# Kernel tuning notes

Measured on AMD Instinct MI355X. Metric: run time of the kernel, lower is better.

## Reference

```python
import jax, jax.numpy as jnp
import numpy as np

B, S, D, H = 4, 2048, 1024, 16
DH = D // H  # 64
EPS = 1e-5


def setup_inputs() -> dict:
    key = jax.random.key(0)
    ks = jax.random.split(key, 6)
    scale = 0.02
    return {
        "x": jax.random.normal(ks[0], (B, S, D), dtype=jnp.float32),
        "Wq": jax.random.normal(ks[1], (H, D, DH), dtype=jnp.float32) * scale,
        "Wk": jax.random.normal(ks[2], (H, D, DH), dtype=jnp.float32) * scale,
        "Wv": jax.random.normal(ks[3], (H, D, DH), dtype=jnp.float32) * scale,
        "Wo": jax.random.normal(ks[4], (D, D), dtype=jnp.float32) * scale,
        "bo": jnp.zeros((D,), dtype=jnp.float32),
        "gamma": jnp.ones((D,), dtype=jnp.float32),
        "beta": jnp.zeros((D,), dtype=jnp.float32),
    }


def reference(x, Wq, Wk, Wv, Wo, bo, gamma, beta):
    # Per-head projections, stacked across heads: [B,H,S,DH]
    q = jnp.einsum("bsd,hdk->bhsk", x, Wq)
    k = jnp.einsum("bsd,hdk->bhsk", x, Wk)
    v = jnp.einsum("bsd,hdk->bhsk", x, Wv)
    inv_scale = 1.0 / jnp.sqrt(jnp.float32(DH))  # key.size(-1) == head_dim
    scores = jnp.einsum("bhqk,bhsk->bhqs", q, k) * inv_scale  # [B,H,S,S]
    attn = jax.nn.softmax(scores, axis=-1)
    ctx = jnp.einsum("bhqs,bhsk->bhqk", attn, v)  # [B,H,S,DH]
    # concat heads -> [B,S,D]
    concat = jnp.transpose(ctx, (0, 2, 1, 3)).reshape(B, S, D)
    proj = concat @ Wo + bo  # fc_out (Wo stored as [in,out])
    added = proj + x  # residual add
    mu = jnp.mean(added, axis=-1, keepdims=True)
    var = jnp.mean(jnp.square(added - mu), axis=-1, keepdims=True)
    normed = (added - mu) * jax.lax.rsqrt(var + EPS)
    return normed * gamma + beta
```

## Files before the change

### kernel.cpp

```cpp
#include <hip/hip_runtime.h>
#include <hip/hip_bf16.h>
#include <stdint.h>

#define DEV __device__ __forceinline__

typedef short s16x8 __attribute__((ext_vector_type(8)));
typedef float f32x4 __attribute__((ext_vector_type(4)));
typedef int i32x4 __attribute__((ext_vector_type(4)));

DEV void async_load16(const void* g, void* l) {
  __builtin_amdgcn_global_load_lds((void __attribute__((address_space(1)))*)(g),
                                   (void __attribute__((address_space(3)))*)(l),
                                   16, 0, 0);
}

DEV unsigned pack_bf16x2(float a, float b) {
  __hip_bfloat162 h = __float22bfloat162_rn(make_float2(a, b));
  union { __hip_bfloat162 h2; unsigned u; } cv;
  cv.h2 = h;
  return cv.u;
}

__global__ __launch_bounds__(256) void cast_x_kernel(const float* __restrict__ in,
                                                     __hip_bfloat16* __restrict__ out, int n4) {
  int i = blockIdx.x * 256 + threadIdx.x;
  if (i >= n4) return;
  float4 v = ((const float4*)in)[i];
  alignas(8) __hip_bfloat16 t[4] = {__float2bfloat16(v.x), __float2bfloat16(v.y),
                                    __float2bfloat16(v.z), __float2bfloat16(v.w)};
  *(uint2*)(out + (size_t)i * 4) = *(const uint2*)t;
}

__global__ __launch_bounds__(256) void transpose_cast_kernel(const float* __restrict__ src,
                                                             __hip_bfloat16* __restrict__ dst,
                                                             int R, int C, float scale) {
  __shared__ float tile[64][65];
  const int r0 = blockIdx.x * 64, c0 = blockIdx.y * 64, bt = blockIdx.z;
  const int tc = threadIdx.x & 63, tr = threadIdx.x >> 6;
  const float* sp = src + (size_t)bt * R * C;
#pragma unroll
  for (int rr = 0; rr < 64; rr += 4)
    tile[tr + rr][tc] = sp[(size_t)(r0 + tr + rr) * C + c0 + tc];
  __syncthreads();
  __hip_bfloat16* dp = dst + (size_t)bt * R * C;
#pragma unroll
  for (int rr = 0; rr < 64; rr += 4) {
    int cc = tr + rr;
    dp[(size_t)(c0 + cc) * R + r0 + tc] = __float2bfloat16(tile[tc][cc] * scale);
  }
}

__global__ __launch_bounds__(256) void qkv_transpose_kernel(const float* __restrict__ Wq,
                                                            const float* __restrict__ Wk,
                                                            const float* __restrict__ Wv,
                                                            __hip_bfloat16* __restrict__ dst,
                                                            float qscale) {
  __shared__ float tile[64][65];
  const int z = blockIdx.z, which = z >> 4, bt = z & 15;
  const int r0 = blockIdx.x * 64;
  const int tc = threadIdx.x & 63, tr = threadIdx.x >> 6;
  const float* src = (which == 0) ? Wq : (which == 1) ? Wk : Wv;
  const float scale = (which == 0) ? qscale : 1.0f;
  const float* sp = src + (size_t)bt * 1024 * 64;
#pragma unroll
  for (int rr = 0; rr < 64; rr += 4)
    tile[tr + rr][tc] = sp[(size_t)(r0 + tr + rr) * 64 + tc];
  __syncthreads();
  __hip_bfloat16* dp = dst + (size_t)z * 1024 * 64;
#pragma unroll
  for (int rr = 0; rr < 64; rr += 4) {
    int cc = tr + rr;
    dp[(size_t)(cc)*1024 + r0 + tc] = __float2bfloat16(tile[tc][cc] * scale);
  }
}

template <int MODE>
__global__ __launch_bounds__(256) void gemm128(const __hip_bfloat16* __restrict__ A,
                                               const __hip_bfloat16* __restrict__ Bt,
                                               void* __restrict__ out0,
                                               void* __restrict__ out1,
                                               void* __restrict__ out2,
                                               const float* __restrict__ bias,
                                               const float* __restrict__ resid,
                                               int M, int N, int K) {
  __shared__ __hip_bfloat16 As[128 * 32];
  __shared__ __hip_bfloat16 Bs[128 * 32];
  const int tid = threadIdx.x;
  const int lane = tid & 63, w = tid >> 6;
  const int lr = lane & 15, lq = lane >> 4;
  const int wm = w >> 1, wn = w & 1;
  const int m0 = blockIdx.y * 128, n0 = blockIdx.x * 128;

  const f32x4 fz = {0.f, 0.f, 0.f, 0.f};
  f32x4 acc[4][4];
#pragma unroll
  for (int i = 0; i < 4; i++)
#pragma unroll
    for (int j = 0; j < 4; j++) acc[i][j] = fz;

  const int kiters = K >> 5;
  for (int kt = 0; kt < kiters; kt++) {
    __syncthreads();
#pragma unroll
    for (int r = 0; r < 2; r++) {
      const int c = r * 256 + tid;
      const int row = c >> 2, kc = c & 3;
      async_load16((const short*)A + (size_t)(m0 + row) * K + kt * 32 + kc * 8,
                   (char*)As + (r * 256 + (tid & 0xC0)) * 16);
      async_load16((const short*)Bt + (size_t)(n0 + row) * K + kt * 32 + kc * 8,
                   (char*)Bs + (r * 256 + (tid & 0xC0)) * 16);
    }
    __syncthreads();
    const short* Ap = (const short*)As;
    const short* Bp = (const short*)Bs;
    s16x8 av[4], bv[4];
#pragma unroll
    for (int i = 0; i < 4; i++)
      av[i] = *(const s16x8*)(Ap + (wm * 64 + i * 16 + lr) * 32 + lq * 8);
#pragma unroll
    for (int j = 0; j < 4; j++)
      bv[j] = *(const s16x8*)(Bp + (wn * 64 + j * 16 + lr) * 32 + lq * 8);
#pragma unroll
    for (int i = 0; i < 4; i++)
#pragma unroll
      for (int j = 0; j < 4; j++)
        acc[i][j] = __builtin_amdgcn_mfma_f32_16x16x32_bf16(av[i], bv[j], acc[i][j], 0, 0, 0);
  }

  if constexpr (MODE == 0) {
    if (n0 < 2048) {
      __hip_bfloat16* dst01 = (__hip_bfloat16*)((n0 < 1024) ? out0 : out1);
#pragma unroll
      for (int i = 0; i < 4; i++)
#pragma unroll
        for (int j = 0; j < 4; j++)
#pragma unroll
          for (int r = 0; r < 4; r++) {
            const int row = m0 + wm * 64 + i * 16 + lq * 4 + r;
            const int col = n0 + wn * 64 + j * 16 + lr;
            const int bb = row >> 11, s = row & 2047;
            const int colq = col & 1023;
            dst01[((((size_t)bb * 16 + (colq >> 6)) * 2048 + s) << 6) + (col & 63)] =
                __float2bfloat16(acc[i][j][r]);
          }
    } else {
#pragma unroll
      for (int i = 0; i < 4; i++)
#pragma unroll
        for (int j = 0; j < 4; j++) {
          const int row0 = m0 + wm * 64 + i * 16 + lq * 4;
          const int col = (n0 - 2048) + wn * 64 + j * 16 + lr;
          const int bb = row0 >> 11, s0 = row0 & 2047;
          alignas(8) __hip_bfloat16 t4[4] = {
              __float2bfloat16(acc[i][j][0]), __float2bfloat16(acc[i][j][1]),
              __float2bfloat16(acc[i][j][2]), __float2bfloat16(acc[i][j][3])};
          *(uint2*)((__hip_bfloat16*)out2 + (size_t)bb * 2097152 + (size_t)col * 2048 + s0) =
              *(const uint2*)t4;
        }
    }
  } else {
#pragma unroll
    for (int i = 0; i < 4; i++)
#pragma unroll
      for (int j = 0; j < 4; j++)
#pragma unroll
        for (int r = 0; r < 4; r++) {
          const int row = m0 + wm * 64 + i * 16 + lq * 4 + r;
          const int col = n0 + wn * 64 + j * 16 + lr;
          const size_t idx = (size_t)row * 1024 + col;
          ((float*)out0)[idx] = acc[i][j][r] + bias[col] + resid[idx];
        }
  }
}

__global__ __launch_bounds__(128, 2) void flash_kernel(const __hip_bfloat16* __restrict__ Qg,
                                                       const __hip_bfloat16* __restrict__ Kg,
                                                       const __hip_bfloat16* __restrict__ Vtg,
                                                       __hip_bfloat16* __restrict__ Og) {
  __shared__ alignas(16) char smem[32768];
  float* xch = (float*)smem;
  const int tid = threadIdx.x;
  const int lane = tid & 63, w = tid >> 6;
  const int lr = lane & 15, lq = lane >> 4;
  const int hb = blockIdx.x, qt = blockIdx.y;
  const int h = hb >> 2, b = hb & 3;
  const size_t bh = (size_t)b * 16 + h;
  const short* Qbase = (const short*)Qg + (bh * 2048 + (size_t)qt * 64) * 64;
  const short* Kbh = (const short*)Kg + bh * 2048 * 64;
  const short* Vbh = (const short*)Vtg + bh * 64 * 2048;

  const int rbase = (lr >> 2) * 8 + (lr & 3);
  const int gk = lr & 7;

  s16x8 qb[4][2];
#pragma unroll
  for (int nt = 0; nt < 4; nt++)
#pragma unroll
    for (int ks = 0; ks < 2; ks++)
      qb[nt][ks] = *(const s16x8*)(Qbase + (nt * 16 + lr) * 64 + ks * 32 + lq * 8);

  s16x8 vones;
#pragma unroll
  for (int e = 0; e < 8; e++) vones[e] = (short)0x3F80;

  const f32x4 fz = {0.f, 0.f, 0.f, 0.f};
  f32x4 o[4][4];
  f32x4 ol[4];
#pragma unroll
  for (int i = 0; i < 4; i++) {
    ol[i] = fz;
#pragma unroll
    for (int j = 0; j < 4; j++) o[i][j] = fz;
  }

  auto stage = [&](int sel, int kb) {
    char* Kl = smem + sel * 16384;
    char* Vl = Kl + 8192;
    const short* Ksrc = Kbh + kb * 64 * 64;
#pragma unroll
    for (int r = 0; r < 4; r++) {
      int c = r * 128 + tid;
      int row = c >> 3, ck = c & 7;
      int g = (row & 3) | (((row >> 3) & 1) << 2);
      async_load16(Ksrc + row * 64 + (ck ^ g) * 8, Kl + (r * 128 + (tid & 64)) * 16);
    }
#pragma unroll
    for (int r = 0; r < 4; r++) {
      int c = r * 128 + tid;
      int row = c >> 3, ck = c & 7;
      async_load16(Vbh + (size_t)row * 2048 + kb * 64 + ((ck ^ (row & 7))) * 8,
                   Vl + (r * 128 + (tid & 64)) * 16);
    }
  };

  stage(0, 0);
  __syncthreads();

  for (int kb = 0; kb < 32; kb++) {
    const int cur = kb & 1;
    if (kb + 1 < 32) stage(cur ^ 1, kb + 1);

    const short* Kp = (const short*)(smem + cur * 16384);
    const short* Vp = (const short*)(smem + cur * 16384 + 8192);

    union { i32x4 i; s16x8 s; } pa[4];
#pragma unroll
    for (int mt = 0; mt < 2; mt++) {
      const int kvrow = w * 32 + mt * 4 + rbase;
      s16x8 kf0 = *(const s16x8*)(Kp + kvrow * 64 + (((0 * 4 + lq) ^ gk)) * 8);
      s16x8 kf1 = *(const s16x8*)(Kp + kvrow * 64 + (((1 * 4 + lq) ^ gk)) * 8);
#pragma unroll
      for (int nt = 0; nt < 4; nt++) {
        f32x4 st = fz;
        st = __builtin_amdgcn_mfma_f32_16x16x32_bf16(kf0, qb[nt][0], st, 0, 0, 0);
        st = __builtin_amdgcn_mfma_f32_16x16x32_bf16(kf1, qb[nt][1], st, 0, 0, 0);
        float e0 = __builtin_amdgcn_exp2f(st[0]);
        float e1 = __builtin_amdgcn_exp2f(st[1]);
        float e2 = __builtin_amdgcn_exp2f(st[2]);
        float e3 = __builtin_amdgcn_exp2f(st[3]);
        pa[nt].i[mt * 2 + 0] = (int)pack_bf16x2(e0, e1);
        pa[nt].i[mt * 2 + 1] = (int)pack_bf16x2(e2, e3);
      }
    }
    __builtin_amdgcn_s_setprio(1);
#pragma unroll
    for (int nt = 0; nt < 4; nt++)
      ol[nt] = __builtin_amdgcn_mfma_f32_16x16x32_bf16(pa[nt].s, vones, ol[nt], 0, 0, 0);
#pragma unroll
    for (int ndh = 0; ndh < 4; ndh++) {
      int vrow = ndh * 16 + lr;
      s16x8 vb = *(const s16x8*)(Vp + vrow * 64 + (((w * 4 + lq) ^ (vrow & 7))) * 8);
#pragma unroll
      for (int nt = 0; nt < 4; nt++)
        o[nt][ndh] = __builtin_amdgcn_mfma_f32_16x16x32_bf16(pa[nt].s, vb, o[nt][ndh], 0, 0, 0);
    }
    __builtin_amdgcn_s_setprio(0);

    __syncthreads();
  }

  __syncthreads();
  if (w == 0) {
#pragma unroll
    for (int j = 0; j < 2; j++) {
#pragma unroll
      for (int ndh = 0; ndh < 4; ndh++)
        *(f32x4*)(xch + 0 * 2560 + (j * 4 + ndh) * 256 + lane * 4) = o[2 + j][ndh];
      *(f32x4*)(xch + 0 * 2560 + 2048 + j * 256 + lane * 4) = ol[2 + j];
    }
  } else {
#pragma unroll
    for (int j = 0; j < 2; j++) {
#pragma unroll
      for (int ndh = 0; ndh < 4; ndh++)
        *(f32x4*)(xch + 1 * 2560 + (j * 4 + ndh) * 256 + lane * 4) = o[0 + j][ndh];
      *(f32x4*)(xch + 1 * 2560 + 2048 + j * 256 + lane * 4) = ol[0 + j];
    }
  }
  __syncthreads();
  if (w == 0) {
#pragma unroll
    for (int j = 0; j < 2; j++) {
#pragma unroll
      for (int ndh = 0; ndh < 4; ndh++)
        o[0 + j][ndh] += *(const f32x4*)(xch + 1 * 2560 + (j * 4 + ndh) * 256 + lane * 4);
      f32x4 lt = ol[0 + j] + *(const f32x4*)(xch + 1 * 2560 + 2048 + j * 256 + lane * 4);
#pragma unroll
      for (int r = 0; r < 4; r++) {
        float inv = __builtin_amdgcn_rcpf(lt[r]);
        int rowg = qt * 64 + (0 + j) * 16 + lq * 4 + r;
#pragma unroll
        for (int ndh = 0; ndh < 4; ndh++)
          Og[((size_t)b * 2048 + rowg) * 1024 + h * 64 + ndh * 16 + lr] =
              __float2bfloat16(o[0 + j][ndh][r] * inv);
      }
    }
  } else {
#pragma unroll
    for (int j = 0; j < 2; j++) {
#pragma unroll
      for (int ndh = 0; ndh < 4; ndh++)
        o[2 + j][ndh] += *(const f32x4*)(xch + 0 * 2560 + (j * 4 + ndh) * 256 + lane * 4);
      f32x4 lt = ol[2 + j] + *(const f32x4*)(xch + 0 * 2560 + 2048 + j * 256 + lane * 4);
#pragma unroll
      for (int r = 0; r < 4; r++) {
        float inv = __builtin_amdgcn_rcpf(lt[r]);
        int rowg = qt * 64 + (2 + j) * 16 + lq * 4 + r;
#pragma unroll
        for (int ndh = 0; ndh < 4; ndh++)
          Og[((size_t)b * 2048 + rowg) * 1024 + h * 64 + ndh * 16 + lr] =
              __float2bfloat16(o[2 + j][ndh][r] * inv);
      }
    }
  }
}

__global__ __launch_bounds__(256) void ln_kernel(const float* __restrict__ tmp,
                                                 const float* __restrict__ gamma,
                                                 const float* __restrict__ beta,
                                                 float* __restrict__ out) {
  const int row = blockIdx.x, tid = threadIdx.x;
  const int lane = tid & 63, w = tid >> 6;
  const float* rp = tmp + (size_t)row * 1024;
  float4 v = ((const float4*)rp)[tid];
  float s = v.x + v.y + v.z + v.w;
  float ss = v.x * v.x + v.y * v.y + v.z * v.z + v.w * v.w;
#pragma unroll
  for (int off = 32; off >= 1; off >>= 1) {
    s += __shfl_xor(s, off);
    ss += __shfl_xor(ss, off);
  }
  __shared__ float red[8];
  if (lane == 0) {
    red[w] = s;
    red[4 + w] = ss;
  }
  __syncthreads();
  s = red[0] + red[1] + red[2] + red[3];
  ss = red[4] + red[5] + red[6] + red[7];
  const float mu = s * (1.0f / 1024.0f);
  const float var = ss * (1.0f / 1024.0f) - mu * mu;
  const float rstd = rsqrtf(var + 1e-5f);
  float4 g = ((const float4*)gamma)[tid];
  float4 be = ((const float4*)beta)[tid];
  float4 ov;
  ov.x = (v.x - mu) * rstd * g.x + be.x;
  ov.y = (v.y - mu) * rstd * g.y + be.y;
  ov.z = (v.z - mu) * rstd * g.z + be.z;
  ov.w = (v.w - mu) * rstd * g.w + be.w;
  ((float4*)(out + (size_t)row * 1024))[tid] = ov;
}

extern "C" void kernel_launch(void* const* d_in, const int* in_sizes, int n_in,
                              void* d_out, int out_size, void* d_ws, size_t ws_size,
                              hipStream_t stream) {
  (void)in_sizes; (void)n_in; (void)out_size; (void)ws_size;
  const float* x = (const float*)d_in[0];
  const float* Wq = (const float*)d_in[1];
  const float* Wk = (const float*)d_in[2];
  const float* Wv = (const float*)d_in[3];
  const float* Wo = (const float*)d_in[4];
  const float* bo = (const float*)d_in[5];
  const float* gamma = (const float*)d_in[6];
  const float* beta = (const float*)d_in[7];
  float* out = (float*)d_out;
  char* ws = (char*)d_ws;

  __hip_bfloat16* xb = (__hip_bfloat16*)(ws + 0);
  __hip_bfloat16* wqkvT = (__hip_bfloat16*)(ws + 16777216);
  __hip_bfloat16* woT = (__hip_bfloat16*)(ws + 23068672);
  __hip_bfloat16* Q = (__hip_bfloat16*)(ws + 25165824);
  __hip_bfloat16* Kt = (__hip_bfloat16*)(ws + 41943040);
  __hip_bfloat16* Vt = (__hip_bfloat16*)(ws + 58720256);
  __hip_bfloat16* cc = (__hip_bfloat16*)(ws + 75497472);
  float* tmp = (float*)(ws + 25165824);

  cast_x_kernel<<<8192, 256, 0, stream>>>(x, xb, 2097152);
  qkv_transpose_kernel<<<dim3(16, 1, 48), 256, 0, stream>>>(Wq, Wk, Wv, wqkvT,
                                                            0.125f * 1.44269504088896f);
  transpose_cast_kernel<<<dim3(16, 16, 1), 256, 0, stream>>>(Wo, woT, 1024, 1024, 1.0f);

  gemm128<0><<<dim3(24, 64), 256, 0, stream>>>(xb, wqkvT, Q, Kt, Vt, nullptr, nullptr,
                                               8192, 3072, 1024);

  flash_kernel<<<dim3(64, 32), 128, 0, stream>>>(Q, Kt, Vt, cc);

  gemm128<2><<<dim3(8, 64), 256, 0, stream>>>(cc, woT, tmp, nullptr, nullptr, bo, x,
                                              8192, 1024, 1024);
  ln_kernel<<<8192, 256, 0, stream>>>(tmp, gamma, beta, out);
}
```

Baseline: 309.1 us.

## Split flash attention work across four waves per block instead of two

```diff
diff --git a/kernel.cpp b/kernel.cpp
--- a/kernel.cpp
+++ b/kernel.cpp
@@ -173,7 +173,7 @@
   }
 }
 
-__global__ __launch_bounds__(128, 2) void flash_kernel(const __hip_bfloat16* __restrict__ Qg,
+__global__ __launch_bounds__(256, 4) void flash_kernel(const __hip_bfloat16* __restrict__ Qg,
                                                        const __hip_bfloat16* __restrict__ Kg,
                                                        const __hip_bfloat16* __restrict__ Vtg,
                                                        __hip_bfloat16* __restrict__ Og) {
@@ -182,6 +182,8 @@
   const int tid = threadIdx.x;
   const int lane = tid & 63, w = tid >> 6;
   const int lr = lane & 15, lq = lane >> 4;
+  const int qp = w >> 1;
+  const int kvh = w & 1;
   const int hb = blockIdx.x, qt = blockIdx.y;
   const int h = hb >> 2, b = hb & 3;
   const size_t bh = (size_t)b * 16 + h;
@@ -192,22 +194,23 @@
   const int rbase = (lr >> 2) * 8 + (lr & 3);
   const int gk = lr & 7;
 
-  s16x8 qb[4][2];
-#pragma unroll
-  for (int nt = 0; nt < 4; nt++)
+  s16x8 qb[2][2];
+#pragma unroll
+  for (int ntl = 0; ntl < 2; ntl++)
 #pragma unroll
     for (int ks = 0; ks < 2; ks++)
-      qb[nt][ks] = *(const s16x8*)(Qbase + (nt * 16 + lr) * 64 + ks * 32 + lq * 8);
+      qb[ntl][ks] =
+          *(const s16x8*)(Qbase + ((qp * 2 + ntl) * 16 + lr) * 64 + ks * 32 + lq * 8);
 
   s16x8 vones;
 #pragma unroll
   for (int e = 0; e < 8; e++) vones[e] = (short)0x3F80;
 
   const f32x4 fz = {0.f, 0.f, 0.f, 0.f};
-  f32x4 o[4][4];
-  f32x4 ol[4];
-#pragma unroll
-  for (int i = 0; i < 4; i++) {
+  f32x4 o[2][4];
+  f32x4 ol[2];
+#pragma unroll
+  for (int i = 0; i < 2; i++) {
     ol[i] = fz;
 #pragma unroll
     for (int j = 0; j < 4; j++) o[i][j] = fz;
@@ -218,18 +221,18 @@
     char* Vl = Kl + 8192;
     const short* Ksrc = Kbh + kb * 64 * 64;
 #pragma unroll
-    for (int r = 0; r < 4; r++) {
-      int c = r * 128 + tid;
+    for (int r = 0; r < 2; r++) {
+      int c = r * 256 + tid;
       int row = c >> 3, ck = c & 7;
       int g = (row & 3) | (((row >> 3) & 1) << 2);
-      async_load16(Ksrc + row * 64 + (ck ^ g) * 8, Kl + (r * 128 + (tid & 64)) * 16);
-    }
-#pragma unroll
-    for (int r = 0; r < 4; r++) {
-      int c = r * 128 + tid;
+      async_load16(Ksrc + row * 64 + (ck ^ g) * 8, Kl + (r * 256 + (tid & 0xC0)) * 16);
+    }
+#pragma unroll
+    for (int r = 0; r < 2; r++) {
+      int c = r * 256 + tid;
       int row = c >> 3, ck = c & 7;
       async_load16(Vbh + (size_t)row * 2048 + kb * 64 + ((ck ^ (row & 7))) * 8,
-                   Vl + (r * 128 + (tid & 64)) * 16);
+                   Vl + (r * 256 + (tid & 0xC0)) * 16);
     }
   };
 
@@ -243,94 +246,84 @@
     const short* Kp = (const short*)(smem + cur * 16384);
     const short* Vp = (const short*)(smem + cur * 16384 + 8192);
 
-    union { i32x4 i; s16x8 s; } pa[4];
+    union { i32x4 i; s16x8 s; } pa[2];
 #pragma unroll
     for (int mt = 0; mt < 2; mt++) {
-      const int kvrow = w * 32 + mt * 4 + rbase;
+      const int kvrow = kvh * 32 + mt * 4 + rbase;
       s16x8 kf0 = *(const s16x8*)(Kp + kvrow * 64 + (((0 * 4 + lq) ^ gk)) * 8);
       s16x8 kf1 = *(const s16x8*)(Kp + kvrow * 64 + (((1 * 4 + lq) ^ gk)) * 8);
 #pragma unroll
-      for (int nt = 0; nt < 4; nt++) {
+      for (int ntl = 0; ntl < 2; ntl++) {
         f32x4 st = fz;
-        st = __builtin_amdgcn_mfma_f32_16x16x32_bf16(kf0, qb[nt][0], st, 0, 0, 0);
-        st = __builtin_amdgcn_mfma_f32_16x16x32_bf16(kf1, qb[nt][1], st, 0, 0, 0);
+        st = __builtin_amdgcn_mfma_f32_16x16x32_bf16(kf0, qb[ntl][0], st, 0, 0, 0);
+        st = __builtin_amdgcn_mfma_f32_16x16x32_bf16(kf1, qb[ntl][1], st, 0, 0, 0);
         float e0 = __builtin_amdgcn_exp2f(st[0]);
         float e1 = __builtin_amdgcn_exp2f(st[1]);
         float e2 = __builtin_amdgcn_exp2f(st[2]);
         float e3 = __builtin_amdgcn_exp2f(st[3]);
-        pa[nt].i[mt * 2 + 0] = (int)pack_bf16x2(e0, e1);
-        pa[nt].i[mt * 2 + 1] = (int)pack_bf16x2(e2, e3);
+        pa[ntl].i[mt * 2 + 0] = (int)pack_bf16x2(e0, e1);
+        pa[ntl].i[mt * 2 + 1] = (int)pack_bf16x2(e2, e3);
       }
     }
     __builtin_amdgcn_s_setprio(1);
 #pragma unroll
-    for (int nt = 0; nt < 4; nt++)
-      ol[nt] = __builtin_amdgcn_mfma_f32_16x16x32_bf16(pa[nt].s, vones, ol[nt], 0, 0, 0);
+    for (int ntl = 0; ntl < 2; ntl++)
+      ol[ntl] = __builtin_amdgcn_mfma_f32_16x16x32_bf16(pa[ntl].s, vones, ol[ntl], 0, 0, 0);
 #pragma unroll
     for (int ndh = 0; ndh < 4; ndh++) {
       int vrow = ndh * 16 + lr;
-      s16x8 vb = *(const s16x8*)(Vp + vrow * 64 + (((w * 4 + lq) ^ (vrow & 7))) * 8);
-#pragma unroll
-      for (int nt = 0; nt < 4; nt++)
-        o[nt][ndh] = __builtin_amdgcn_mfma_f32_16x16x32_bf16(pa[nt].s, vb, o[nt][ndh], 0, 0, 0);
+      s16x8 vb = *(const s16x8*)(Vp + vrow * 64 + (((kvh * 4 + lq) ^ (vrow & 7))) * 8);
+#pragma unroll
+      for (int ntl = 0; ntl < 2; ntl++)
+        o[ntl][ndh] =
+            __builtin_amdgcn_mfma_f32_16x16x32_bf16(pa[ntl].s, vb, o[ntl][ndh], 0, 0, 0);
     }
     __builtin_amdgcn_s_setprio(0);
 
     __syncthreads();
   }
 
+  float* slot = xch + w * 1280;
+  if (kvh == 0) {
+#pragma unroll
+    for (int ndh = 0; ndh < 4; ndh++)
+      *(f32x4*)(slot + ndh * 256 + lane * 4) = o[1][ndh];
+    *(f32x4*)(slot + 1024 + lane * 4) = ol[1];
+  } else {
+#pragma unroll
+    for (int ndh = 0; ndh < 4; ndh++)
+      *(f32x4*)(slot + ndh * 256 + lane * 4) = o[0][ndh];
+    *(f32x4*)(slot + 1024 + lane * 4) = ol[0];
+  }
   __syncthreads();
-  if (w == 0) {
-#pragma unroll
-    for (int j = 0; j < 2; j++) {
+  const float* ps = xch + (w ^ 1) * 1280;
+  if (kvh == 0) {
+#pragma unroll
+    for (int ndh = 0; ndh < 4; ndh++)
+      o[0][ndh] += *(const f32x4*)(ps + ndh * 256 + lane * 4);
+    f32x4 lt = ol[0] + *(const f32x4*)(ps + 1024 + lane * 4);
+#pragma unroll
+    for (int r = 0; r < 4; r++) {
+      float inv = __builtin_amdgcn_rcpf(lt[r]);
+      int rowg = qt * 64 + w * 16 + lq * 4 + r;
 #pragma unroll
       for (int ndh = 0; ndh < 4; ndh++)
-        *(f32x4*)(xch + 0 * 2560 + (j * 4 + ndh) * 256 + lane * 4) = o[2 + j][ndh];
-      *(f32x4*)(xch + 0 * 2560 + 2048 + j * 256 + lane * 4) = ol[2 + j];
+        Og[((size_t)b * 2048 + rowg) * 1024 + h * 64 + ndh * 16 + lr] =
+            __float2bfloat16(o[0][ndh][r] * inv);
     }
   } else {
 #pragma unroll
-    for (int j = 0; j < 2; j++) {
+    for (int ndh = 0; ndh < 4; ndh++)
+      o[1][ndh] += *(const f32x4*)(ps + ndh * 256 + lane * 4);
+    f32x4 lt = ol[1] + *(const f32x4*)(ps + 1024 + lane * 4);
+#pragma unroll
+    for (int r = 0; r < 4; r++) {
+      float inv = __builtin_amdgcn_rcpf(lt[r]);
+      int rowg = qt * 64 + w * 16 + lq * 4 + r;
 #pragma unroll
       for (int ndh = 0; ndh < 4; ndh++)
-        *(f32x4*)(xch + 1 * 2560 + (j * 4 + ndh) * 256 + lane * 4) = o[0 + j][ndh];
-      *(f32x4*)(xch + 1 * 2560 + 2048 + j * 256 + lane * 4) = ol[0 + j];
-    }
-  }
-  __syncthreads();
-  if (w == 0) {
-#pragma unroll
-    for (int j = 0; j < 2; j++) {
-#pragma unroll
-      for (int ndh = 0; ndh < 4; ndh++)
-        o[0 + j][ndh] += *(const f32x4*)(xch + 1 * 2560 + (j * 4 + ndh) * 256 + lane * 4);
-      f32x4 lt = ol[0 + j] + *(const f32x4*)(xch + 1 * 2560 + 2048 + j * 256 + lane * 4);
-#pragma unroll
-      for (int r = 0; r < 4; r++) {
-        float inv = __builtin_amdgcn_rcpf(lt[r]);
-        int rowg = qt * 64 + (0 + j) * 16 + lq * 4 + r;
-#pragma unroll
-        for (int ndh = 0; ndh < 4; ndh++)
-          Og[((size_t)b * 2048 + rowg) * 1024 + h * 64 + ndh * 16 + lr] =
-              __float2bfloat16(o[0 + j][ndh][r] * inv);
-      }
-    }
-  } else {
-#pragma unroll
-    for (int j = 0; j < 2; j++) {
-#pragma unroll
-      for (int ndh = 0; ndh < 4; ndh++)
-        o[2 + j][ndh] += *(const f32x4*)(xch + 0 * 2560 + (j * 4 + ndh) * 256 + lane * 4);
-      f32x4 lt = ol[2 + j] + *(const f32x4*)(xch + 0 * 2560 + 2048 + j * 256 + lane * 4);
-#pragma unroll
-      for (int r = 0; r < 4; r++) {
-        float inv = __builtin_amdgcn_rcpf(lt[r]);
-        int rowg = qt * 64 + (2 + j) * 16 + lq * 4 + r;
-#pragma unroll
-        for (int ndh = 0; ndh < 4; ndh++)
-          Og[((size_t)b * 2048 + rowg) * 1024 + h * 64 + ndh * 16 + lr] =
-              __float2bfloat16(o[2 + j][ndh][r] * inv);
-      }
+        Og[((size_t)b * 2048 + rowg) * 1024 + h * 64 + ndh * 16 + lr] =
+            __float2bfloat16(o[1][ndh][r] * inv);
     }
   }
 }
@@ -403,7 +396,7 @@
   gemm128<0><<<dim3(24, 64), 256, 0, stream>>>(xb, wqkvT, Q, Kt, Vt, nullptr, nullptr,
                                                8192, 3072, 1024);
 
-  flash_kernel<<<dim3(64, 32), 128, 0, stream>>>(Q, Kt, Vt, cc);
+  flash_kernel<<<dim3(64, 32), 256, 0, stream>>>(Q, Kt, Vt, cc);
 
   gemm128<2><<<dim3(8, 64), 256, 0, stream>>>(cc, woT, tmp, nullptr, nullptr, bo, x,
                                               8192, 1024, 1024);
```

New measurement: 307.3 us. No clear change (-0.6%).
